# Kernel optimization log

Measured on AMD Instinct MI355X. Metric: run time of the kernel, lower is better.

## Reference

```python
import jax, jax.numpy as jnp
import numpy as np

S = 17          # number of segment ids (0 = background, skipped)
MIN_H = 100.0   # HomographySmoothLoss.min_segment_pixels
MIN_V = 50.0    # ObjectVarianceLoss.min_segment_pixels
SUPPRESS = 0.1  # BoundaryAwareSmoothLoss.boundary_suppress


def _maxpool3(x):
    # torch F.max_pool2d(k=3, stride=1, pad=1) pads with -inf
    return jax.lax.reduce_window(x, -jnp.inf, jax.lax.max,
                                 (1, 1, 3, 3), (1, 1, 1, 1),
                                 ((0, 0), (0, 0), (1, 1), (1, 1)))


def _boundary_map(masks):
    lab = masks.astype(jnp.float32)[:, None]  # (B,1,H,W)
    dil = _maxpool3(lab)
    ero = -_maxpool3(-lab)
    return (dil != ero).astype(jnp.float32)


def _nearest(x, Ho, Wo):
    # torch F.interpolate(mode='nearest'): src = floor(dst * in/out)
    H, W = x.shape[-2], x.shape[-1]
    yi = (jnp.arange(Ho) * H) // Ho
    xi = (jnp.arange(Wo) * W) // Wo
    return x[..., yi, :][..., :, xi]


def _conv3(x, k):
    return jax.lax.conv_general_dilated(x, k, (1, 1), ((1, 1), (1, 1)),
                                        dimension_numbers=('NCHW', 'OIHW', 'NCHW'))


def _segment_losses(flow, masks):
    # Vectorized replacement of per-(batch,segment) python loops:
    # accumulate per-segment moments with segment_sum, then batched 3x3
    # normal-equation solves (equivalent to torch.lstsq affine fit).
    B, _, H, W = flow.shape
    NS = B * S
    xs = jnp.broadcast_to(jnp.arange(W, dtype=jnp.float32)[None, None, :], (B, H, W)).reshape(-1)
    ys = jnp.broadcast_to(jnp.arange(H, dtype=jnp.float32)[None, :, None], (B, H, W)).reshape(-1)
    u = flow[:, 0].reshape(-1)
    v = flow[:, 1].reshape(-1)
    seg = masks.reshape(-1)
    bidx = jnp.repeat(jnp.arange(B, dtype=jnp.int32), H * W)
    idx = bidx * S + seg                                  # global segment id
    ones = jnp.ones_like(xs)
    feats = jnp.stack([ones, xs, ys, xs * xs, xs * ys, ys * ys,
                       u, v, u * u, v * v, xs * u, ys * u, xs * v, ys * v], axis=1)
    sums = jax.ops.segment_sum(feats, idx, num_segments=NS)  # (NS,14)
    (n, Sx, Sy, Sxx, Sxy, Syy, Su, Sv, Suu, Svv,
     Sxu, Syu, Sxv, Syv) = [sums[:, i] for i in range(14)]
    segids = jnp.tile(jnp.arange(S), B)

    # ---- homography loss: per-segment affine least-squares fit ----
    valid_h = (segids != 0) & (n >= MIN_H)
    ATA = jnp.stack([jnp.stack([Sxx, Sxy, Sx], -1),
                     jnp.stack([Sxy, Syy, Sy], -1),
                     jnp.stack([Sx, Sy, n], -1)], axis=1)   # (NS,3,3)
    eye3 = jnp.eye(3, dtype=flow.dtype)
    ATA = jnp.where(valid_h[:, None, None], ATA, eye3)      # keep solve nonsingular
    ATb = jnp.stack([jnp.stack([Sxu, Sxv], -1),
                     jnp.stack([Syu, Syv], -1),
                     jnp.stack([Su, Sv], -1)], axis=1)      # (NS,3,2)
    ATb = jnp.where(valid_h[:, None, None], ATb, 0.0)
    params = jnp.linalg.solve(ATA, ATb)                     # (NS,3,2): [a,b,c] for u and v
    p = params[idx]                                         # (BHW,3,2) gather per pixel
    pred_u = xs * p[:, 0, 0] + ys * p[:, 1, 0] + p[:, 2, 0]
    pred_v = xs * p[:, 0, 1] + ys * p[:, 1, 1] + p[:, 2, 1]
    res = jnp.sqrt((u - pred_u) ** 2 + (v - pred_v) ** 2)
    res_mean = jax.ops.segment_sum(res, idx, num_segments=NS) / jnp.maximum(n, 1.0)
    nh = jnp.maximum(jnp.sum(valid_h), 1)
    homog = jnp.sum(res_mean * valid_h) / nh

    # ---- object variance loss (unbiased var, matches torch .var()) ----
    valid_v = (segids != 0) & (n >= MIN_V)
    nsafe = jnp.maximum(n, 2.0)
    var_u = (Suu - Su * Su / nsafe) / (nsafe - 1.0)
    var_v = (Svv - Sv * Sv / nsafe) / (nsafe - 1.0)
    nv = jnp.maximum(jnp.sum(valid_v), 1)
    ovar = jnp.sum((var_u + var_v) * valid_v) / nv
    return homog, ovar


def setup_inputs():
    key = jax.random.key(0)
    k1, k2, k3 = jax.random.split(key, 3)
    B, H, W = 8, 512, 1024
    flow = jax.random.normal(k1, (B, 2, H, W), jnp.float32)
    masks = jax.random.randint(k2, (B, H, W), 0, S).astype(jnp.int32)
    images = jax.random.uniform(k3, (B, 3, H, W), jnp.float32)
    return {"flow": flow, "masks": masks, "images": images}


def reference(flow, masks, images):
    boundary = _boundary_map(masks)                         # (B,1,H,W)
    homog, ovar = _segment_losses(flow, masks)

    # ---- boundary sharpness (sobel on flow magnitude) ----
    sobel_x = jnp.array([[-1., 0., 1.], [-2., 0., 2.], [-1., 0., 1.]], jnp.float32).reshape(1, 1, 3, 3)
    sobel_y = jnp.array([[-1., -2., -1.], [0., 0., 0.], [1., 2., 1.]], jnp.float32).reshape(1, 1, 3, 3)
    flow_mag = jnp.sqrt(jnp.sum(flow ** 2, axis=1, keepdims=True))
    fg = jnp.abs(_conv3(flow_mag, sobel_x)) + jnp.abs(_conv3(flow_mag, sobel_y))
    fg = fg / (jnp.max(fg) + 1e-6)
    bn = boundary / (jnp.max(boundary) + 1e-6)
    sharp = jnp.mean(bn * (1.0 - fg))

    # ---- boundary-aware edge-weighted smoothness ----
    flow_dx = flow[:, :, :, 1:] - flow[:, :, :, :-1]
    flow_dy = flow[:, :, 1:, :] - flow[:, :, :-1, :]
    g = jnp.mean(images, axis=1, keepdims=True)
    wx = jnp.exp(-jnp.abs(g[:, :, :, 1:] - g[:, :, :, :-1]) * 10.0)
    wy = jnp.exp(-jnp.abs(g[:, :, 1:, :] - g[:, :, :-1, :]) * 10.0)
    bx = _nearest(boundary, wx.shape[2], wx.shape[3])
    by = _nearest(boundary, wy.shape[2], wy.shape[3])
    wx = wx * (1.0 - (1.0 - SUPPRESS) * bx)
    wy = wy * (1.0 - (1.0 - SUPPRESS) * by)
    smooth = jnp.mean(jnp.abs(flow_dx) * wx) + jnp.mean(jnp.abs(flow_dy) * wy)

    # weights all 1.0; order: homography, boundary_sharpness, object_variance, boundary_smooth
    return jnp.stack([homog, sharp, ovar, smooth])
```

## Files before the change

kernel.cpp:

```cpp
#include <hip/hip_runtime.h>
#include <math.h>

#define BB 8
#define HH 512
#define WW 1024
#define HW (HH * WW)
#define NPIX (BB * HW)
#define NSEG 16
#define SUPPRESS 0.1f


__device__ __forceinline__ float wave_sum(float t) {
    #pragma unroll
    for (int off = 32; off > 0; off >>= 1) t += __shfl_down(t, off);
    return t;
}

#define REP8(M) M(0) M(1) M(2) M(3) M(4) M(5) M(6) M(7)

__global__ __launch_bounds__(256) void moments_kernel(
    const float* __restrict__ flow,
    const int*   __restrict__ masks,
    double* __restrict__ moments4)
{
    __shared__ float bins[9984];

    const int tid  = threadIdx.x;
    const int lane = tid & 63;
    const int wid  = tid >> 6;
    const int bid  = blockIdx.x;
    const int colg = bid & 15;
    const int rowg = (bid >> 4) & 7;
    const int b    = bid >> 7;
    const int par  = bid & 3;

    const int c0 = colg * 64;
    const int r0 = rowg * 64;

    const float* fu = flow + (long long)b * (2LL * HW);
    const float* fv = fu + HW;
    const int*   mk = masks + (long long)b * HW;
    const int*   mrow = mk + r0 * WW + c0 + lane;
    const float* urow = fu + r0 * WW + c0 + lane;
    const float* vrow = fv + r0 * WW + c0 + lane;

    for (int i = tid; i < 2496; i += 256)
        *(float4*)&bins[i * 4] = make_float4(0.f, 0.f, 0.f, 0.f);
    __syncthreads();

    int   m0 = mrow[0];
    float u0 = urow[0], v0 = vrow[0];
    int   m1 = mrow[WW];
    float u1 = urow[WW], v1 = vrow[WW];

#define MPROC(RR, MM, UU, VV) { \
    const float y = (float)(r0 + (RR)); \
    float* bp = &bins[(MM) * 576 + lane]; \
    if (wid == 0) { \
        float b0 = bp[0], b1 = bp[64], b2 = bp[128]; \
        b0 += 1.f; b1 += y; b2 = fmaf(y, y, b2); \
        bp[0] = b0; bp[64] = b1; bp[128] = b2; \
    } else if (wid == 1) { \
        float b3 = bp[192], b5 = bp[320]; \
        b3 += (UU); b5 = fmaf((UU), (UU), b5); \
        bp[192] = b3; bp[320] = b5; \
    } else if (wid == 2) { \
        float b4 = bp[256], b6 = bp[384]; \
        b4 += (VV); b6 = fmaf((VV), (VV), b6); \
        bp[256] = b4; bp[384] = b6; \
    } else { \
        float b7 = bp[448], b8 = bp[512]; \
        b7 = fmaf(y, (UU), b7); b8 = fmaf(y, (VV), b8); \
        bp[448] = b7; bp[512] = b8; \
    } }

    #pragma unroll 1
    for (int r = 0; r < 64; r += 2) {
        const int o2 = ((r + 2) & 63) * WW;
        const int o3 = ((r + 3) & 63) * WW;
        const int   m2 = mrow[o2];
        const float u2 = urow[o2], v2 = vrow[o2];
        const int   m3 = mrow[o3];
        const float u3 = urow[o3], v3 = vrow[o3];

        MPROC(r, m0, u0, v0)
        MPROC(r + 1, m1, u1, v1)

        m0 = m2; u0 = u2; v0 = v2;
        m1 = m3; u1 = u3; v1 = v3;
    }
    __syncthreads();

    const unsigned long long SRC = 0x84736543210100ULL;
    const unsigned long long PW  = 0x01010000012010ULL;
    double* cell = moments4 + par * 1792 + b * 224;
    {
        const int p   = tid;
        const int act = (p < 224);
        const int pc  = act ? p : 0;
        const int segm = pc / 14;
        const int feat = pc - segm * 14;
        const int srcb = (int)((SRC >> (4 * feat)) & 15);
        const int pw   = (int)((PW  >> (4 * feat)) & 15);
        const float* bp = &bins[(segm + 1) * 576 + srcb * 64];
        float acc = 0.f;
        #pragma unroll 8
        for (int l0 = 0; l0 < 64; ++l0) {
            const int l = (l0 + lane) & 63;
            const float xv = (float)(c0 + l);
            const float w = (pw == 0) ? 1.f : ((pw == 1) ? xv : xv * xv);
            acc = fmaf(bp[l], w, acc);
        }
        if (act) atomicAdd(&cell[segm * 14 + feat], (double)acc);
    }
}

__global__ __launch_bounds__(256) void stencil_kernel(
    const float* __restrict__ flow,
    const int*   __restrict__ masks,
    const float* __restrict__ images,
    double* __restrict__ scal64,
    unsigned* __restrict__ maxfg64)
{
    __shared__ float    smX[4][260], smW[4][260];
    __shared__ unsigned mX[4][260],  mW[4][260];
    __shared__ float    gX[2][260];
    __shared__ float    ue[2][260],  ve[2][260];
    __shared__ float    wred[4][5];

    const int tid = threadIdx.x;
    const int lane = tid & 63;
    const long long base = (long long)blockIdx.x * 2048;
    const int b  = (int)(base >> 19);
    const int h0 = (int)((base & (HW - 1)) >> 10);

    const float* fu = flow + (long long)b * (2LL * HW);
    const float* fv = fu + HW;
    const int*   mk = masks + (long long)b * HW;
    const float* i0 = images + (long long)b * (3LL * HW);
    const float* i1 = i0 + HW;
    const float* i2 = i1 + HW;

    const int c4 = tid * 4;
    float4 m4a[4];
    unsigned mbp[4];
    float4 ur[3], vr[3];
    float4 gr[3];

    #pragma unroll
    for (int r = 0; r < 4; ++r) {
        const int grow = h0 - 1 + r;
        const int mr = grow < 0 ? 0 : (grow > HH - 1 ? HH - 1 : grow);
        const int4 mv = *(const int4*)&mk[mr * WW + c4];
        mbp[r] = (unsigned)(mv.x & 255) | ((unsigned)(mv.y & 255) << 8) |
                 ((unsigned)(mv.z & 255) << 16) | ((unsigned)(mv.w & 255) << 24);

        float4 u4 = make_float4(0.f, 0.f, 0.f, 0.f);
        float4 v4 = make_float4(0.f, 0.f, 0.f, 0.f);
        if (grow >= 0 && grow <= HH - 1) {
            u4 = *(const float4*)&fu[grow * WW + c4];
            v4 = *(const float4*)&fv[grow * WW + c4];
        }
        float4 m4;
        m4.x = sqrtf(u4.x * u4.x + v4.x * v4.x);
        m4.y = sqrtf(u4.y * u4.y + v4.y * v4.y);
        m4.z = sqrtf(u4.z * u4.z + v4.z * v4.z);
        m4.w = sqrtf(u4.w * u4.w + v4.w * v4.w);
        m4a[r] = m4;
        smX[r][tid] = m4.x;
        smW[r][tid + 1] = m4.w;
        mX[r][tid] = (unsigned)(mv.x & 255);
        mW[r][tid + 1] = (unsigned)(mv.w & 255);
        if (tid == 0)   { smW[r][0] = 0.f;   mW[r][0] = (unsigned)(mv.x & 255); }
        if (tid == 255) { smX[r][256] = 0.f; mX[r][256] = (unsigned)(mv.w & 255); }
        if (r >= 1) { ur[r - 1] = u4; vr[r - 1] = v4; }
    }
    #pragma unroll
    for (int r = 0; r < 3; ++r) {
        const int grow = h0 + r;
        float4 g4 = make_float4(0.f, 0.f, 0.f, 0.f);
        if (grow <= HH - 1) {
            const float4 a  = *(const float4*)&i0[grow * WW + c4];
            const float4 bq = *(const float4*)&i1[grow * WW + c4];
            const float4 c  = *(const float4*)&i2[grow * WW + c4];
            g4.x = (a.x + bq.x + c.x) * (1.f / 3.f);
            g4.y = (a.y + bq.y + c.y) * (1.f / 3.f);
            g4.z = (a.z + bq.z + c.z) * (1.f / 3.f);
            g4.w = (a.w + bq.w + c.w) * (1.f / 3.f);
        }
        gr[r] = g4;
        if (r < 2) gX[r][tid] = g4.x;
    }
    ue[0][tid] = ur[0].x; ve[0][tid] = vr[0].x;
    ue[1][tid] = ur[1].x; ve[1][tid] = vr[1].x;
    __syncthreads();

    float a_dx = 0.f, a_dy = 0.f, a_sb = 0.f, a_sbf = 0.f, mfg = 0.f;

    #pragma unroll
    for (int lr = 0; lr < 2; ++lr) {
        const int h = h0 + lr;
        float a[3][6];
        unsigned long long kw[3];
        #pragma unroll
        for (int r = 0; r < 3; ++r) {
            const int rr = lr + r;
            const float4 own = m4a[rr];
            a[r][0] = smW[rr][tid];
            a[r][1] = own.x; a[r][2] = own.y; a[r][3] = own.z; a[r][4] = own.w;
            a[r][5] = smX[rr][tid + 1];
            kw[r] = (unsigned long long)mW[rr][tid]
                  | ((unsigned long long)mbp[rr] << 8)
                  | ((unsigned long long)mX[rr][tid + 1] << 40);
        }
        const float4 gc = gr[lr];
        const float4 gd4 = gr[lr + 1];
        const float gval[5] = {gc.x, gc.y, gc.z, gc.w, gX[lr][tid + 1]};
        const float gd[4]  = {gd4.x, gd4.y, gd4.z, gd4.w};
        const float4 uc4 = ur[lr],  vc4 = vr[lr];
        const float4 ud4 = ur[lr + 1], vd4 = vr[lr + 1];
        const float uc[5] = {uc4.x, uc4.y, uc4.z, uc4.w, ue[lr][tid + 1]};
        const float vc[5] = {vc4.x, vc4.y, vc4.z, vc4.w, ve[lr][tid + 1]};
        const float ud[4] = {ud4.x, ud4.y, ud4.z, ud4.w};
        const float vd[4] = {vd4.x, vd4.y, vd4.z, vd4.w};

        #pragma unroll
        for (int j = 0; j < 4; ++j) {
            const int w = c4 + j;
            const unsigned cseg = (unsigned)((kw[1] >> (8 * (j + 1))) & 255);
            int bnd = (((kw[0] >> (8 * j)) & 255) != cseg)
                    | (((kw[0] >> (8 * (j + 1))) & 255) != cseg)
                    | (((kw[0] >> (8 * (j + 2))) & 255) != cseg)
                    | (((kw[1] >> (8 * j)) & 255) != cseg)
                    | (((kw[1] >> (8 * (j + 2))) & 255) != cseg)
                    | (((kw[2] >> (8 * j)) & 255) != cseg)
                    | (((kw[2] >> (8 * (j + 1))) & 255) != cseg)
                    | (((kw[2] >> (8 * (j + 2))) & 255) != cseg);

            const float fgx = (a[0][j + 2] - a[0][j]) + 2.f * (a[1][j + 2] - a[1][j]) +
                              (a[2][j + 2] - a[2][j]);
            const float fgy = (a[2][j] + 2.f * a[2][j + 1] + a[2][j + 2]) -
                              (a[0][j] + 2.f * a[0][j + 1] + a[0][j + 2]);
            const float fgraw = fabsf(fgx) + fabsf(fgy);
            mfg = fmaxf(mfg, fgraw);
            if (bnd) { a_sb += 1.f; a_sbf += fgraw; }

            const float u = uc[j], v = vc[j], g0 = gval[j];
            if (w < WW - 1) {
                const float wgt = expf(-fabsf(gval[j + 1] - g0) * 10.f) * (bnd ? SUPPRESS : 1.f);
                a_dx += (fabsf(uc[j + 1] - u) + fabsf(vc[j + 1] - v)) * wgt;
            }
            if (h < HH - 1) {
                const float wgt = expf(-fabsf(gd[j] - g0) * 10.f) * (bnd ? SUPPRESS : 1.f);
                a_dy += (fabsf(ud[j] - u) + fabsf(vd[j] - v)) * wgt;
            }
        }
    }

    for (int off = 32; off > 0; off >>= 1) {
        a_dx += __shfl_down(a_dx, off);
        a_dy += __shfl_down(a_dy, off);
        a_sb += __shfl_down(a_sb, off);
        a_sbf += __shfl_down(a_sbf, off);
        mfg = fmaxf(mfg, __shfl_down(mfg, off));
    }
    if (lane == 0) {
        const int wv = tid >> 6;
        wred[wv][0] = a_dx; wred[wv][1] = a_dy; wred[wv][2] = a_sb;
        wred[wv][3] = a_sbf; wred[wv][4] = mfg;
    }
    __syncthreads();
    if (tid == 0) {
        float dx = 0.f, dy = 0.f, sb = 0.f, sbf = 0.f, mf = 0.f;
        for (int i = 0; i < 4; ++i) {
            dx += wred[i][0]; dy += wred[i][1]; sb += wred[i][2];
            sbf += wred[i][3]; mf = fmaxf(mf, wred[i][4]);
        }
        const int sl = blockIdx.x & 63;
        atomicAdd(&scal64[sl * 4 + 0], (double)dx);
        atomicAdd(&scal64[sl * 4 + 1], (double)dy);
        atomicAdd(&scal64[sl * 4 + 2], (double)sb);
        atomicAdd(&scal64[sl * 4 + 3], (double)sbf);
        atomicMax(&maxfg64[sl], __float_as_uint(mf));
    }
}

__global__ __launch_bounds__(128) void solve_kernel(
    const double* __restrict__ moments4,
    float* __restrict__ params,
    int* __restrict__ valid,
    float* __restrict__ out)
{
    const int i = threadIdx.x;
    double m[14];
    #pragma unroll
    for (int k = 0; k < 14; ++k) {
        double s = 0.0;
        #pragma unroll
        for (int par = 0; par < 4; ++par) s += moments4[par * 1792 + i * 14 + k];
        m[k] = s;
    }
    const double n = m[0];
    const int vh = (n >= 100.0) ? 1 : 0;
    float p[6] = {0.f, 0.f, 0.f, 0.f, 0.f, 0.f};
    if (vh) {
        double A[3][3] = {{m[3], m[4], m[1]},
                          {m[4], m[5], m[2]},
                          {m[1], m[2], n}};
        double Bm[3][2] = {{m[10], m[12]},
                           {m[11], m[13]},
                           {m[6],  m[7]}};
        for (int k = 0; k < 3; ++k) {
            int piv = k; double mx = fabs(A[k][k]);
            for (int r = k + 1; r < 3; ++r) {
                double a = fabs(A[r][k]);
                if (a > mx) { mx = a; piv = r; }
            }
            if (piv != k) {
                for (int c = 0; c < 3; ++c) { double t = A[k][c]; A[k][c] = A[piv][c]; A[piv][c] = t; }
                for (int c = 0; c < 2; ++c) { double t = Bm[k][c]; Bm[k][c] = Bm[piv][c]; Bm[piv][c] = t; }
            }
            const double inv = 1.0 / A[k][k];
            for (int r = k + 1; r < 3; ++r) {
                const double f = A[r][k] * inv;
                for (int c = k; c < 3; ++c) A[r][c] -= f * A[k][c];
                Bm[r][0] -= f * Bm[k][0];
                Bm[r][1] -= f * Bm[k][1];
            }
        }
        double X[3][2];
        for (int c = 0; c < 2; ++c) {
            X[2][c] = Bm[2][c] / A[2][2];
            X[1][c] = (Bm[1][c] - A[1][2] * X[2][c]) / A[1][1];
            X[0][c] = (Bm[0][c] - A[0][1] * X[1][c] - A[0][2] * X[2][c]) / A[0][0];
        }
        p[0] = (float)X[0][0]; p[1] = (float)X[1][0]; p[2] = (float)X[2][0];
        p[3] = (float)X[0][1]; p[4] = (float)X[1][1]; p[5] = (float)X[2][1];
    }
    valid[i] = vh;
    for (int c = 0; c < 6; ++c) params[i * 6 + c] = p[c];

    const int vv = (n >= 50.0) ? 1 : 0;
    double var = 0.0;
    if (vv) {
        const double ns = (n > 2.0) ? n : 2.0;
        const double var_u = (m[8] - m[6] * m[6] / ns) / (ns - 1.0);
        const double var_v = (m[9] - m[7] * m[7] / ns) / (ns - 1.0);
        var = var_u + var_v;
    }
    __shared__ double svar[128];
    __shared__ int scnt[128];
    svar[i] = var; scnt[i] = vv;
    __syncthreads();
    for (int s = 64; s > 0; s >>= 1) {
        if (i < s) { svar[i] += svar[i + s]; scnt[i] += scnt[i + s]; }
        __syncthreads();
    }
    if (i == 0) out[2] = (float)(svar[0] / (double)(scnt[0] > 1 ? scnt[0] : 1));
}

__global__ __launch_bounds__(256) void pass2_kernel(
    const float* __restrict__ flow,
    const int*   __restrict__ masks,
    const float* __restrict__ params,
    double* __restrict__ res4)
{
    __shared__ float sp[17 * 6];

    const long long base = (long long)blockIdx.x * 4096;
    const int b      = (int)(base >> 19);
    const int hwbase = (int)(base & (HW - 1));
    const int tid    = threadIdx.x;
    const int lane   = tid & 63;

    if (tid < 6) sp[tid] = 0.f;
    if (tid < 96) sp[6 + tid] = params[b * 96 + tid];
    __syncthreads();

    const float* fu = flow + (long long)b * (2LL * HW);
    const float* fv = fu + HW;
    const int*   mk = masks + (long long)b * HW;

#define DECLR(i) float r_##i = 0.f;
    REP8(DECLR)
#define DECLR2(i) float q_##i = 0.f;
    REP8(DECLR2)

    #pragma unroll
    for (int it = 0; it < 4; ++it) {
        const int i4 = hwbase + it * 1024 + tid * 4;
        const int4   m4 = *(const int4*)&mk[i4];
        const float4 u4 = *(const float4*)&fu[i4];
        const float4 v4 = *(const float4*)&fv[i4];
        const int segs[4] = {m4.x, m4.y, m4.z, m4.w};
        const float us[4] = {u4.x, u4.y, u4.z, u4.w};
        const float vs[4] = {v4.x, v4.y, v4.z, v4.w};
        #pragma unroll
        for (int j = 0; j < 4; ++j) {
            const int seg = segs[j];
            const float* pf = &sp[seg * 6];
            const int hw = i4 + j;
            const float x = (float)(hw & 1023), y = (float)((hw & (HW - 1)) >> 10);
            const float du = us[j] - (x * pf[0] + y * pf[1] + pf[2]);
            const float dv = vs[j] - (x * pf[3] + y * pf[4] + pf[5]);
            const float r = sqrtf(du * du + dv * dv);
            const int sr = seg - 1;
#define STEPR(i) r_##i += (sr == i) ? r : 0.f;
            REP8(STEPR)
#define STEPR2(i) q_##i += (sr == 8 + i) ? r : 0.f;
            REP8(STEPR2)
        }
    }

    const int par = blockIdx.x & 3;
    double* rb = &res4[par * 128 + b * 16];
#define FINR(i) { const float s = wave_sum(r_##i); \
    if (lane == 0) atomicAdd(rb + i, (double)s); }
    REP8(FINR)
#define FINR2(i) { const float s = wave_sum(q_##i); \
    if (lane == 0) atomicAdd(rb + 8 + i, (double)s); }
    REP8(FINR2)
}

__global__ __launch_bounds__(128) void final_kernel(
    const double* __restrict__ moments4,
    const double* __restrict__ res4,
    const int*    __restrict__ valid,
    const double* __restrict__ scal64,
    const unsigned* __restrict__ maxfg64,
    float* __restrict__ out)
{
    const int i = threadIdx.x;
    double n = 0.0, rs = 0.0;
    #pragma unroll
    for (int par = 0; par < 4; ++par) {
        n  += moments4[par * 1792 + i * 14];
        rs += res4[par * 128 + i];
    }
    const int vh = valid[i];
    const double rm = vh ? rs / (n > 1.0 ? n : 1.0) : 0.0;
    __shared__ double sr[128];
    __shared__ int sc[128];
    sr[i] = rm; sc[i] = vh;
    __syncthreads();
    for (int s = 64; s > 0; s >>= 1) {
        if (i < s) { sr[i] += sr[i + s]; sc[i] += sc[i + s]; }
        __syncthreads();
    }
    if (i == 0) {
        out[0] = (float)(sr[0] / (double)(sc[0] > 1 ? sc[0] : 1));
        double dx = 0.0, dy = 0.0, sb = 0.0, sbf = 0.0;
        float mf = 0.f;
        for (int k = 0; k < 64; ++k) {
            dx += scal64[k * 4 + 0]; dy += scal64[k * 4 + 1];
            sb += scal64[k * 4 + 2]; sbf += scal64[k * 4 + 3];
            mf = fmaxf(mf, __uint_as_float(maxfg64[k]));
        }
        const double maxfg = (double)mf;
        const double maxb = (sb > 0.0) ? 1.0 : 0.0;
        out[1] = (float)((sb - sbf / (maxfg + 1e-6)) / (maxb + 1e-6) / (double)NPIX);
        const double smooth = dx / (double)(2LL * BB * HH * (WW - 1)) +
                              dy / (double)(2LL * BB * (HH - 1) * WW);
        out[3] = (float)smooth;
    }
}

extern "C" void kernel_launch(void* const* d_in, const int* in_sizes, int n_in,
                              void* d_out, int out_size, void* d_ws, size_t ws_size,
                              hipStream_t stream)
{
    const float* flow   = (const float*)d_in[0];
    const int*   masks  = (const int*)d_in[1];
    const float* images = (const float*)d_in[2];
    float* out = (float*)d_out;

    char* ws = (char*)d_ws;
    double*   moments4 = (double*)(ws);
    double*   res4     = (double*)(ws + 57344);
    double*   scal64   = (double*)(ws + 61440);
    unsigned* maxfg64  = (unsigned*)(ws + 63488);
    float*    params   = (float*)(ws + 63744);
    int*      valid    = (int*)(ws + 66816);

    hipMemsetAsync(d_ws, 0, 67584, stream);

    moments_kernel<<<dim3(1024), dim3(256), 0, stream>>>(flow, masks, moments4);
    stencil_kernel<<<dim3(NPIX / 2048), dim3(256), 0, stream>>>(
        flow, masks, images, scal64, maxfg64);
    solve_kernel<<<dim3(1), dim3(128), 0, stream>>>(moments4, params, valid, out);
    pass2_kernel<<<dim3(NPIX / 4096), dim3(256), 0, stream>>>(
        flow, masks, params, res4);
    final_kernel<<<dim3(1), dim3(128), 0, stream>>>(
        moments4, res4, valid, scal64, maxfg64, out);
}
```

Baseline: 108.8 us.

## Fuse affine residual pass into stencil kernel after the solve

```diff
diff --git a/kernel.cpp b/kernel.cpp
--- a/kernel.cpp
+++ b/kernel.cpp
@@ -115,176 +115,6 @@
     }
 }
 
-__global__ __launch_bounds__(256) void stencil_kernel(
-    const float* __restrict__ flow,
-    const int*   __restrict__ masks,
-    const float* __restrict__ images,
-    double* __restrict__ scal64,
-    unsigned* __restrict__ maxfg64)
-{
-    __shared__ float    smX[4][260], smW[4][260];
-    __shared__ unsigned mX[4][260],  mW[4][260];
-    __shared__ float    gX[2][260];
-    __shared__ float    ue[2][260],  ve[2][260];
-    __shared__ float    wred[4][5];
-
-    const int tid = threadIdx.x;
-    const int lane = tid & 63;
-    const long long base = (long long)blockIdx.x * 2048;
-    const int b  = (int)(base >> 19);
-    const int h0 = (int)((base & (HW - 1)) >> 10);
-
-    const float* fu = flow + (long long)b * (2LL * HW);
-    const float* fv = fu + HW;
-    const int*   mk = masks + (long long)b * HW;
-    const float* i0 = images + (long long)b * (3LL * HW);
-    const float* i1 = i0 + HW;
-    const float* i2 = i1 + HW;
-
-    const int c4 = tid * 4;
-    float4 m4a[4];
-    unsigned mbp[4];
-    float4 ur[3], vr[3];
-    float4 gr[3];
-
-    #pragma unroll
-    for (int r = 0; r < 4; ++r) {
-        const int grow = h0 - 1 + r;
-        const int mr = grow < 0 ? 0 : (grow > HH - 1 ? HH - 1 : grow);
-        const int4 mv = *(const int4*)&mk[mr * WW + c4];
-        mbp[r] = (unsigned)(mv.x & 255) | ((unsigned)(mv.y & 255) << 8) |
-                 ((unsigned)(mv.z & 255) << 16) | ((unsigned)(mv.w & 255) << 24);
-
-        float4 u4 = make_float4(0.f, 0.f, 0.f, 0.f);
-        float4 v4 = make_float4(0.f, 0.f, 0.f, 0.f);
-        if (grow >= 0 && grow <= HH - 1) {
-            u4 = *(const float4*)&fu[grow * WW + c4];
-            v4 = *(const float4*)&fv[grow * WW + c4];
-        }
-        float4 m4;
-        m4.x = sqrtf(u4.x * u4.x + v4.x * v4.x);
-        m4.y = sqrtf(u4.y * u4.y + v4.y * v4.y);
-        m4.z = sqrtf(u4.z * u4.z + v4.z * v4.z);
-        m4.w = sqrtf(u4.w * u4.w + v4.w * v4.w);
-        m4a[r] = m4;
-        smX[r][tid] = m4.x;
-        smW[r][tid + 1] = m4.w;
-        mX[r][tid] = (unsigned)(mv.x & 255);
-        mW[r][tid + 1] = (unsigned)(mv.w & 255);
-        if (tid == 0)   { smW[r][0] = 0.f;   mW[r][0] = (unsigned)(mv.x & 255); }
-        if (tid == 255) { smX[r][256] = 0.f; mX[r][256] = (unsigned)(mv.w & 255); }
-        if (r >= 1) { ur[r - 1] = u4; vr[r - 1] = v4; }
-    }
-    #pragma unroll
-    for (int r = 0; r < 3; ++r) {
-        const int grow = h0 + r;
-        float4 g4 = make_float4(0.f, 0.f, 0.f, 0.f);
-        if (grow <= HH - 1) {
-            const float4 a  = *(const float4*)&i0[grow * WW + c4];
-            const float4 bq = *(const float4*)&i1[grow * WW + c4];
-            const float4 c  = *(const float4*)&i2[grow * WW + c4];
-            g4.x = (a.x + bq.x + c.x) * (1.f / 3.f);
-            g4.y = (a.y + bq.y + c.y) * (1.f / 3.f);
-            g4.z = (a.z + bq.z + c.z) * (1.f / 3.f);
-            g4.w = (a.w + bq.w + c.w) * (1.f / 3.f);
-        }
-        gr[r] = g4;
-        if (r < 2) gX[r][tid] = g4.x;
-    }
-    ue[0][tid] = ur[0].x; ve[0][tid] = vr[0].x;
-    ue[1][tid] = ur[1].x; ve[1][tid] = vr[1].x;
-    __syncthreads();
-
-    float a_dx = 0.f, a_dy = 0.f, a_sb = 0.f, a_sbf = 0.f, mfg = 0.f;
-
-    #pragma unroll
-    for (int lr = 0; lr < 2; ++lr) {
-        const int h = h0 + lr;
-        float a[3][6];
-        unsigned long long kw[3];
-        #pragma unroll
-        for (int r = 0; r < 3; ++r) {
-            const int rr = lr + r;
-            const float4 own = m4a[rr];
-            a[r][0] = smW[rr][tid];
-            a[r][1] = own.x; a[r][2] = own.y; a[r][3] = own.z; a[r][4] = own.w;
-            a[r][5] = smX[rr][tid + 1];
-            kw[r] = (unsigned long long)mW[rr][tid]
-                  | ((unsigned long long)mbp[rr] << 8)
-                  | ((unsigned long long)mX[rr][tid + 1] << 40);
-        }
-        const float4 gc = gr[lr];
-        const float4 gd4 = gr[lr + 1];
-        const float gval[5] = {gc.x, gc.y, gc.z, gc.w, gX[lr][tid + 1]};
-        const float gd[4]  = {gd4.x, gd4.y, gd4.z, gd4.w};
-        const float4 uc4 = ur[lr],  vc4 = vr[lr];
-        const float4 ud4 = ur[lr + 1], vd4 = vr[lr + 1];
-        const float uc[5] = {uc4.x, uc4.y, uc4.z, uc4.w, ue[lr][tid + 1]};
-        const float vc[5] = {vc4.x, vc4.y, vc4.z, vc4.w, ve[lr][tid + 1]};
-        const float ud[4] = {ud4.x, ud4.y, ud4.z, ud4.w};
-        const float vd[4] = {vd4.x, vd4.y, vd4.z, vd4.w};
-
-        #pragma unroll
-        for (int j = 0; j < 4; ++j) {
-            const int w = c4 + j;
-            const unsigned cseg = (unsigned)((kw[1] >> (8 * (j + 1))) & 255);
-            int bnd = (((kw[0] >> (8 * j)) & 255) != cseg)
-                    | (((kw[0] >> (8 * (j + 1))) & 255) != cseg)
-                    | (((kw[0] >> (8 * (j + 2))) & 255) != cseg)
-                    | (((kw[1] >> (8 * j)) & 255) != cseg)
-                    | (((kw[1] >> (8 * (j + 2))) & 255) != cseg)
-                    | (((kw[2] >> (8 * j)) & 255) != cseg)
-                    | (((kw[2] >> (8 * (j + 1))) & 255) != cseg)
-                    | (((kw[2] >> (8 * (j + 2))) & 255) != cseg);
-
-            const float fgx = (a[0][j + 2] - a[0][j]) + 2.f * (a[1][j + 2] - a[1][j]) +
-                              (a[2][j + 2] - a[2][j]);
-            const float fgy = (a[2][j] + 2.f * a[2][j + 1] + a[2][j + 2]) -
-                              (a[0][j] + 2.f * a[0][j + 1] + a[0][j + 2]);
-            const float fgraw = fabsf(fgx) + fabsf(fgy);
-            mfg = fmaxf(mfg, fgraw);
-            if (bnd) { a_sb += 1.f; a_sbf += fgraw; }
-
-            const float u = uc[j], v = vc[j], g0 = gval[j];
-            if (w < WW - 1) {
-                const float wgt = expf(-fabsf(gval[j + 1] - g0) * 10.f) * (bnd ? SUPPRESS : 1.f);
-                a_dx += (fabsf(uc[j + 1] - u) + fabsf(vc[j + 1] - v)) * wgt;
-            }
-            if (h < HH - 1) {
-                const float wgt = expf(-fabsf(gd[j] - g0) * 10.f) * (bnd ? SUPPRESS : 1.f);
-                a_dy += (fabsf(ud[j] - u) + fabsf(vd[j] - v)) * wgt;
-            }
-        }
-    }
-
-    for (int off = 32; off > 0; off >>= 1) {
-        a_dx += __shfl_down(a_dx, off);
-        a_dy += __shfl_down(a_dy, off);
-        a_sb += __shfl_down(a_sb, off);
-        a_sbf += __shfl_down(a_sbf, off);
-        mfg = fmaxf(mfg, __shfl_down(mfg, off));
-    }
-    if (lane == 0) {
-        const int wv = tid >> 6;
-        wred[wv][0] = a_dx; wred[wv][1] = a_dy; wred[wv][2] = a_sb;
-        wred[wv][3] = a_sbf; wred[wv][4] = mfg;
-    }
-    __syncthreads();
-    if (tid == 0) {
-        float dx = 0.f, dy = 0.f, sb = 0.f, sbf = 0.f, mf = 0.f;
-        for (int i = 0; i < 4; ++i) {
-            dx += wred[i][0]; dy += wred[i][1]; sb += wred[i][2];
-            sbf += wred[i][3]; mf = fmaxf(mf, wred[i][4]);
-        }
-        const int sl = blockIdx.x & 63;
-        atomicAdd(&scal64[sl * 4 + 0], (double)dx);
-        atomicAdd(&scal64[sl * 4 + 1], (double)dy);
-        atomicAdd(&scal64[sl * 4 + 2], (double)sb);
-        atomicAdd(&scal64[sl * 4 + 3], (double)sbf);
-        atomicMax(&maxfg64[sl], __float_as_uint(mf));
-    }
-}
-
 __global__ __launch_bounds__(128) void solve_kernel(
     const double* __restrict__ moments4,
     float* __restrict__ params,
@@ -359,59 +189,183 @@
     if (i == 0) out[2] = (float)(svar[0] / (double)(scnt[0] > 1 ? scnt[0] : 1));
 }
 
-__global__ __launch_bounds__(256) void pass2_kernel(
+__global__ __launch_bounds__(256, 4) void stencil_kernel(
     const float* __restrict__ flow,
     const int*   __restrict__ masks,
+    const float* __restrict__ images,
     const float* __restrict__ params,
+    double* __restrict__ scal64,
+    unsigned* __restrict__ maxfg64,
     double* __restrict__ res4)
 {
-    __shared__ float sp[17 * 6];
-
-    const long long base = (long long)blockIdx.x * 4096;
-    const int b      = (int)(base >> 19);
-    const int hwbase = (int)(base & (HW - 1));
-    const int tid    = threadIdx.x;
-    const int lane   = tid & 63;
-
-    if (tid < 6) sp[tid] = 0.f;
-    if (tid < 96) sp[6 + tid] = params[b * 96 + tid];
-    __syncthreads();
+    __shared__ float    smX[4][260], smW[4][260];
+    __shared__ unsigned mX[4][260],  mW[4][260];
+    __shared__ float    gX[2][260];
+    __shared__ float    ue[2][260],  ve[2][260];
+    __shared__ float    sp[17 * 6];
+    __shared__ float    wred[4][5];
+
+    const int tid = threadIdx.x;
+    const int lane = tid & 63;
+    const long long base = (long long)blockIdx.x * 2048;
+    const int b  = (int)(base >> 19);
+    const int h0 = (int)((base & (HW - 1)) >> 10);
 
     const float* fu = flow + (long long)b * (2LL * HW);
     const float* fv = fu + HW;
     const int*   mk = masks + (long long)b * HW;
-
+    const float* i0 = images + (long long)b * (3LL * HW);
+    const float* i1 = i0 + HW;
+    const float* i2 = i1 + HW;
+
+    if (tid < 6) sp[tid] = 0.f;
+    if (tid < 96) sp[6 + tid] = params[b * 96 + tid];
+
+    const int c4 = tid * 4;
+    float4 m4a[4];
+    unsigned mbp[4];
+    float4 ur[3], vr[3];
+    float4 gr[3];
+
+    #pragma unroll
+    for (int r = 0; r < 4; ++r) {
+        const int grow = h0 - 1 + r;
+        const int mr = grow < 0 ? 0 : (grow > HH - 1 ? HH - 1 : grow);
+        const int4 mv = *(const int4*)&mk[mr * WW + c4];
+        mbp[r] = (unsigned)(mv.x & 255) | ((unsigned)(mv.y & 255) << 8) |
+                 ((unsigned)(mv.z & 255) << 16) | ((unsigned)(mv.w & 255) << 24);
+
+        float4 u4 = make_float4(0.f, 0.f, 0.f, 0.f);
+        float4 v4 = make_float4(0.f, 0.f, 0.f, 0.f);
+        if (grow >= 0 && grow <= HH - 1) {
+            u4 = *(const float4*)&fu[grow * WW + c4];
+            v4 = *(const float4*)&fv[grow * WW + c4];
+        }
+        float4 m4;
+        m4.x = sqrtf(u4.x * u4.x + v4.x * v4.x);
+        m4.y = sqrtf(u4.y * u4.y + v4.y * v4.y);
+        m4.z = sqrtf(u4.z * u4.z + v4.z * v4.z);
+        m4.w = sqrtf(u4.w * u4.w + v4.w * v4.w);
+        m4a[r] = m4;
+        smX[r][tid] = m4.x;
+        smW[r][tid + 1] = m4.w;
+        mX[r][tid] = (unsigned)(mv.x & 255);
+        mW[r][tid + 1] = (unsigned)(mv.w & 255);
+        if (tid == 0)   { smW[r][0] = 0.f;   mW[r][0] = (unsigned)(mv.x & 255); }
+        if (tid == 255) { smX[r][256] = 0.f; mX[r][256] = (unsigned)(mv.w & 255); }
+        if (r >= 1) { ur[r - 1] = u4; vr[r - 1] = v4; }
+    }
+    #pragma unroll
+    for (int r = 0; r < 3; ++r) {
+        const int grow = h0 + r;
+        float4 g4 = make_float4(0.f, 0.f, 0.f, 0.f);
+        if (grow <= HH - 1) {
+            const float4 a  = *(const float4*)&i0[grow * WW + c4];
+            const float4 bq = *(const float4*)&i1[grow * WW + c4];
+            const float4 c  = *(const float4*)&i2[grow * WW + c4];
+            g4.x = (a.x + bq.x + c.x) * (1.f / 3.f);
+            g4.y = (a.y + bq.y + c.y) * (1.f / 3.f);
+            g4.z = (a.z + bq.z + c.z) * (1.f / 3.f);
+            g4.w = (a.w + bq.w + c.w) * (1.f / 3.f);
+        }
+        gr[r] = g4;
+        if (r < 2) gX[r][tid] = g4.x;
+    }
+    ue[0][tid] = ur[0].x; ve[0][tid] = vr[0].x;
+    ue[1][tid] = ur[1].x; ve[1][tid] = vr[1].x;
+    __syncthreads();
+
+    float a_dx = 0.f, a_dy = 0.f, a_sb = 0.f, a_sbf = 0.f, mfg = 0.f;
 #define DECLR(i) float r_##i = 0.f;
     REP8(DECLR)
 #define DECLR2(i) float q_##i = 0.f;
     REP8(DECLR2)
 
     #pragma unroll
-    for (int it = 0; it < 4; ++it) {
-        const int i4 = hwbase + it * 1024 + tid * 4;
-        const int4   m4 = *(const int4*)&mk[i4];
-        const float4 u4 = *(const float4*)&fu[i4];
-        const float4 v4 = *(const float4*)&fv[i4];
-        const int segs[4] = {m4.x, m4.y, m4.z, m4.w};
-        const float us[4] = {u4.x, u4.y, u4.z, u4.w};
-        const float vs[4] = {v4.x, v4.y, v4.z, v4.w};
+    for (int lr = 0; lr < 2; ++lr) {
+        const int h = h0 + lr;
+        float a[3][6];
+        unsigned long long kw[3];
+        #pragma unroll
+        for (int r = 0; r < 3; ++r) {
+            const int rr = lr + r;
+            const float4 own = m4a[rr];
+            a[r][0] = smW[rr][tid];
+            a[r][1] = own.x; a[r][2] = own.y; a[r][3] = own.z; a[r][4] = own.w;
+            a[r][5] = smX[rr][tid + 1];
+            kw[r] = (unsigned long long)mW[rr][tid]
+                  | ((unsigned long long)mbp[rr] << 8)
+                  | ((unsigned long long)mX[rr][tid + 1] << 40);
+        }
+        const float4 gc = gr[lr];
+        const float4 gd4 = gr[lr + 1];
+        const float gval[5] = {gc.x, gc.y, gc.z, gc.w, gX[lr][tid + 1]};
+        const float gd[4]  = {gd4.x, gd4.y, gd4.z, gd4.w};
+        const float4 uc4 = ur[lr],  vc4 = vr[lr];
+        const float4 ud4 = ur[lr + 1], vd4 = vr[lr + 1];
+        const float uc[5] = {uc4.x, uc4.y, uc4.z, uc4.w, ue[lr][tid + 1]};
+        const float vc[5] = {vc4.x, vc4.y, vc4.z, vc4.w, ve[lr][tid + 1]};
+        const float ud[4] = {ud4.x, ud4.y, ud4.z, ud4.w};
+        const float vd[4] = {vd4.x, vd4.y, vd4.z, vd4.w};
+
         #pragma unroll
         for (int j = 0; j < 4; ++j) {
-            const int seg = segs[j];
-            const float* pf = &sp[seg * 6];
-            const int hw = i4 + j;
-            const float x = (float)(hw & 1023), y = (float)((hw & (HW - 1)) >> 10);
-            const float du = us[j] - (x * pf[0] + y * pf[1] + pf[2]);
-            const float dv = vs[j] - (x * pf[3] + y * pf[4] + pf[5]);
-            const float r = sqrtf(du * du + dv * dv);
-            const int sr = seg - 1;
-#define STEPR(i) r_##i += (sr == i) ? r : 0.f;
-            REP8(STEPR)
-#define STEPR2(i) q_##i += (sr == 8 + i) ? r : 0.f;
-            REP8(STEPR2)
-        }
-    }
-
+            const int w = c4 + j;
+            const unsigned cseg = (unsigned)((kw[1] >> (8 * (j + 1))) & 255);
+            int bnd = (((kw[0] >> (8 * j)) & 255) != cseg)
+                    | (((kw[0] >> (8 * (j + 1))) & 255) != cseg)
+                    | (((kw[0] >> (8 * (j + 2))) & 255) != cseg)
+                    | (((kw[1] >> (8 * j)) & 255) != cseg)
+                    | (((kw[1] >> (8 * (j + 2))) & 255) != cseg)
+                    | (((kw[2] >> (8 * j)) & 255) != cseg)
+                    | (((kw[2] >> (8 * (j + 1))) & 255) != cseg)
+                    | (((kw[2] >> (8 * (j + 2))) & 255) != cseg);
+
+            const float fgx = (a[0][j + 2] - a[0][j]) + 2.f * (a[1][j + 2] - a[1][j]) +
+                              (a[2][j + 2] - a[2][j]);
+            const float fgy = (a[2][j] + 2.f * a[2][j + 1] + a[2][j + 2]) -
+                              (a[0][j] + 2.f * a[0][j + 1] + a[0][j + 2]);
+            const float fgraw = fabsf(fgx) + fabsf(fgy);
+            mfg = fmaxf(mfg, fgraw);
+            if (bnd) { a_sb += 1.f; a_sbf += fgraw; }
+
+            const float u = uc[j], v = vc[j], g0 = gval[j];
+            if (w < WW - 1) {
+                const float wgt = expf(-fabsf(gval[j + 1] - g0) * 10.f) * (bnd ? SUPPRESS : 1.f);
+                a_dx += (fabsf(uc[j + 1] - u) + fabsf(vc[j + 1] - v)) * wgt;
+            }
+            if (h < HH - 1) {
+                const float wgt = expf(-fabsf(gd[j] - g0) * 10.f) * (bnd ? SUPPRESS : 1.f);
+                a_dy += (fabsf(ud[j] - u) + fabsf(vd[j] - v)) * wgt;
+            }
+
+            {
+                const float* pf = &sp[cseg * 6];
+                const float x = (float)w, y = (float)h;
+                const float du = u - (x * pf[0] + y * pf[1] + pf[2]);
+                const float dv = v - (x * pf[3] + y * pf[4] + pf[5]);
+                const float rres = sqrtf(du * du + dv * dv);
+                const int sr = (int)cseg - 1;
+#define STEPR(i) r_##i += (sr == i) ? rres : 0.f;
+                REP8(STEPR)
+#define STEPR2(i) q_##i += (sr == 8 + i) ? rres : 0.f;
+                REP8(STEPR2)
+            }
+        }
+    }
+
+    for (int off = 32; off > 0; off >>= 1) {
+        a_dx += __shfl_down(a_dx, off);
+        a_dy += __shfl_down(a_dy, off);
+        a_sb += __shfl_down(a_sb, off);
+        a_sbf += __shfl_down(a_sbf, off);
+        mfg = fmaxf(mfg, __shfl_down(mfg, off));
+    }
+    if (lane == 0) {
+        const int wv = tid >> 6;
+        wred[wv][0] = a_dx; wred[wv][1] = a_dy; wred[wv][2] = a_sb;
+        wred[wv][3] = a_sbf; wred[wv][4] = mfg;
+    }
     const int par = blockIdx.x & 3;
     double* rb = &res4[par * 128 + b * 16];
 #define FINR(i) { const float s = wave_sum(r_##i); \
@@ -420,6 +374,21 @@
 #define FINR2(i) { const float s = wave_sum(q_##i); \
     if (lane == 0) atomicAdd(rb + 8 + i, (double)s); }
     REP8(FINR2)
+
+    __syncthreads();
+    if (tid == 0) {
+        float dx = 0.f, dy = 0.f, sb = 0.f, sbf = 0.f, mf = 0.f;
+        for (int i = 0; i < 4; ++i) {
+            dx += wred[i][0]; dy += wred[i][1]; sb += wred[i][2];
+            sbf += wred[i][3]; mf = fmaxf(mf, wred[i][4]);
+        }
+        const int sl = blockIdx.x & 63;
+        atomicAdd(&scal64[sl * 4 + 0], (double)dx);
+        atomicAdd(&scal64[sl * 4 + 1], (double)dy);
+        atomicAdd(&scal64[sl * 4 + 2], (double)sb);
+        atomicAdd(&scal64[sl * 4 + 3], (double)sbf);
+        atomicMax(&maxfg64[sl], __float_as_uint(mf));
+    }
 }
 
 __global__ __launch_bounds__(128) void final_kernel(
@@ -485,11 +454,9 @@
     hipMemsetAsync(d_ws, 0, 67584, stream);
 
     moments_kernel<<<dim3(1024), dim3(256), 0, stream>>>(flow, masks, moments4);
+    solve_kernel<<<dim3(1), dim3(128), 0, stream>>>(moments4, params, valid, out);
     stencil_kernel<<<dim3(NPIX / 2048), dim3(256), 0, stream>>>(
-        flow, masks, images, scal64, maxfg64);
-    solve_kernel<<<dim3(1), dim3(128), 0, stream>>>(moments4, params, valid, out);
-    pass2_kernel<<<dim3(NPIX / 4096), dim3(256), 0, stream>>>(
-        flow, masks, params, res4);
+        flow, masks, images, params, scal64, maxfg64, res4);
     final_kernel<<<dim3(1), dim3(128), 0, stream>>>(
         moments4, res4, valid, scal64, maxfg64, out);
 }
```

Result: slower. 226.8 us (+108.5%).

## Merge moments and stencil kernels into one interleaved launch

Applied to the files above, without the earlier changes.

```diff
diff --git a/kernel.cpp b/kernel.cpp
--- a/kernel.cpp
+++ b/kernel.cpp
@@ -18,17 +18,14 @@
 
 #define REP8(M) M(0) M(1) M(2) M(3) M(4) M(5) M(6) M(7)
 
-__global__ __launch_bounds__(256) void moments_kernel(
-    const float* __restrict__ flow,
-    const int*   __restrict__ masks,
-    double* __restrict__ moments4)
-{
-    __shared__ float bins[9984];
-
+
+__device__ void moments_body(
+    const float* __restrict__ flow, const int* __restrict__ masks,
+    double* __restrict__ moments4, float* bins, int bid)
+{
     const int tid  = threadIdx.x;
     const int lane = tid & 63;
     const int wid  = tid >> 6;
-    const int bid  = blockIdx.x;
     const int colg = bid & 15;
     const int rowg = (bid >> 4) & 7;
     const int b    = bid >> 7;
@@ -115,22 +112,24 @@
     }
 }
 
-__global__ __launch_bounds__(256) void stencil_kernel(
-    const float* __restrict__ flow,
-    const int*   __restrict__ masks,
+__device__ void stencil_body(
+    const float* __restrict__ flow, const int* __restrict__ masks,
     const float* __restrict__ images,
-    double* __restrict__ scal64,
-    unsigned* __restrict__ maxfg64)
-{
-    __shared__ float    smX[4][260], smW[4][260];
-    __shared__ unsigned mX[4][260],  mW[4][260];
-    __shared__ float    gX[2][260];
-    __shared__ float    ue[2][260],  ve[2][260];
-    __shared__ float    wred[4][5];
+    double* __restrict__ scal64, unsigned* __restrict__ maxfg64,
+    char* smem, int bid)
+{
+    float    (*smX)[260] = (float (*)[260])(smem);
+    float    (*smW)[260] = (float (*)[260])(smem + 4160);
+    unsigned (*mX)[260]  = (unsigned (*)[260])(smem + 8320);
+    unsigned (*mW)[260]  = (unsigned (*)[260])(smem + 12480);
+    float    (*gX)[260]  = (float (*)[260])(smem + 16640);
+    float    (*ue)[260]  = (float (*)[260])(smem + 18720);
+    float    (*ve)[260]  = (float (*)[260])(smem + 20800);
+    float    (*wred)[5]  = (float (*)[5])(smem + 22880);
 
     const int tid = threadIdx.x;
     const int lane = tid & 63;
-    const long long base = (long long)blockIdx.x * 2048;
+    const long long base = (long long)bid * 2048;
     const int b  = (int)(base >> 19);
     const int h0 = (int)((base & (HW - 1)) >> 10);
 
@@ -276,12 +275,30 @@
             dx += wred[i][0]; dy += wred[i][1]; sb += wred[i][2];
             sbf += wred[i][3]; mf = fmaxf(mf, wred[i][4]);
         }
-        const int sl = blockIdx.x & 63;
+        const int sl = bid & 63;
         atomicAdd(&scal64[sl * 4 + 0], (double)dx);
         atomicAdd(&scal64[sl * 4 + 1], (double)dy);
         atomicAdd(&scal64[sl * 4 + 2], (double)sb);
         atomicAdd(&scal64[sl * 4 + 3], (double)sbf);
         atomicMax(&maxfg64[sl], __float_as_uint(mf));
+    }
+}
+
+__global__ __launch_bounds__(256) void uber_kernel(
+    const float* __restrict__ flow,
+    const int*   __restrict__ masks,
+    const float* __restrict__ images,
+    double* __restrict__ moments4,
+    double* __restrict__ scal64,
+    unsigned* __restrict__ maxfg64)
+{
+    __shared__ char smem[39936];
+    const int bid = blockIdx.x;
+    if ((bid % 3) == 2) {
+        moments_body(flow, masks, moments4, (float*)smem, bid / 3);
+    } else {
+        stencil_body(flow, masks, images, scal64, maxfg64, smem,
+                     (bid / 3) * 2 + (bid % 3));
     }
 }
 
@@ -484,9 +501,8 @@
 
     hipMemsetAsync(d_ws, 0, 67584, stream);
 
-    moments_kernel<<<dim3(1024), dim3(256), 0, stream>>>(flow, masks, moments4);
-    stencil_kernel<<<dim3(NPIX / 2048), dim3(256), 0, stream>>>(
-        flow, masks, images, scal64, maxfg64);
+    uber_kernel<<<dim3(3072), dim3(256), 0, stream>>>(
+        flow, masks, images, moments4, scal64, maxfg64);
     solve_kernel<<<dim3(1), dim3(128), 0, stream>>>(moments4, params, valid, out);
     pass2_kernel<<<dim3(NPIX / 4096), dim3(256), 0, stream>>>(
         flow, masks, params, res4);
```

Result: faster. 106.5 us (median of 3 runs) (-2.1%).
